# Performance work log

Hardware: AMD Instinct MI355X
Metric: run time of the kernel (lower is better)

The kernel has to match this reference:

```python
import jax, jax.numpy as jnp
import numpy as np

H = 64
NUM_HEADS = 4
NUM_LAYERS = 2
B = 524288
EPS = 1e-5


def _layernorm(x, g, b):
    mu = jnp.mean(x, axis=-1, keepdims=True)
    var = jnp.mean((x - mu) ** 2, axis=-1, keepdims=True)
    return (x - mu) * jax.lax.rsqrt(var + EPS) * g + b


def _mha(x, w_qkv, b_qkv, w_o, b_o):
    # x: (B, M, H). Fused in-proj like torch nn.MultiheadAttention.
    Bx, M, Hx = x.shape
    hd = Hx // NUM_HEADS
    qkv = x @ w_qkv.T + b_qkv                      # (B, M, 3H)
    q, k, v = jnp.split(qkv, 3, axis=-1)
    q = q.reshape(Bx, M, NUM_HEADS, hd)
    k = k.reshape(Bx, M, NUM_HEADS, hd)
    v = v.reshape(Bx, M, NUM_HEADS, hd)
    scores = jnp.einsum('bqnd,bknd->bnqk', q, k) / jnp.sqrt(jnp.asarray(hd, x.dtype))
    a = jax.nn.softmax(scores, axis=-1)
    o = jnp.einsum('bnqk,bknd->bqnd', a, v).reshape(Bx, M, Hx)
    return o @ w_o.T + b_o


def _block(x, rel, p):
    attn_out = _mha(x, p['w_qkv'], p['b_qkv'], p['w_o'], p['b_o'])
    attn_out = attn_out * rel[:, :, None]
    x = _layernorm(x + attn_out, p['n1_g'], p['n1_b'])
    ffn = jax.nn.relu(x @ p['ffn_w'].T + p['ffn_b'])
    return _layernorm(x + ffn, p['n2_g'], p['n2_b'])


def setup_inputs() -> dict:
    key = jax.random.key(0)
    ks = jax.random.split(key, 32)
    inp = {
        'h_poi': jax.random.normal(ks[0], (B, H), jnp.float32),
        'h_census': jax.random.normal(ks[1], (B, H), jnp.float32),
        'h_traffic': jax.random.normal(ks[2], (B, H), jnp.float32),
        'mfr_poi': jax.random.uniform(ks[3], (B, 2), jnp.float32),
        'mfr_census': jax.random.uniform(ks[4], (B, 2), jnp.float32),
        'mfr_traffic': jax.random.uniform(ks[5], (B, 2), jnp.float32),
        'rel_w': jax.random.normal(ks[6], (1, 2), jnp.float32) * 0.5,
        'rel_b': jnp.zeros((1,), jnp.float32),
    }
    s = 1.0 / np.sqrt(H)
    for l in range(NUM_LAYERS):
        kk = jax.random.split(ks[7 + l], 6)
        inp[f'l{l}_w_qkv'] = jax.random.normal(kk[0], (3 * H, H), jnp.float32) * s
        inp[f'l{l}_b_qkv'] = jnp.zeros((3 * H,), jnp.float32)
        inp[f'l{l}_w_o'] = jax.random.normal(kk[1], (H, H), jnp.float32) * s
        inp[f'l{l}_b_o'] = jnp.zeros((H,), jnp.float32)
        inp[f'l{l}_ffn_w'] = jax.random.normal(kk[2], (H, H), jnp.float32) * s
        inp[f'l{l}_ffn_b'] = jnp.zeros((H,), jnp.float32)
        inp[f'l{l}_n1_g'] = jnp.ones((H,), jnp.float32)
        inp[f'l{l}_n1_b'] = jnp.zeros((H,), jnp.float32)
        inp[f'l{l}_n2_g'] = jnp.ones((H,), jnp.float32)
        inp[f'l{l}_n2_b'] = jnp.zeros((H,), jnp.float32)
    return inp


def reference(h_poi, h_census, h_traffic, mfr_poi, mfr_census, mfr_traffic,
              rel_w, rel_b,
              l0_w_qkv, l0_b_qkv, l0_w_o, l0_b_o, l0_ffn_w, l0_ffn_b,
              l0_n1_g, l0_n1_b, l0_n2_g, l0_n2_b,
              l1_w_qkv, l1_b_qkv, l1_w_o, l1_b_o, l1_ffn_w, l1_ffn_b,
              l1_n1_g, l1_n1_b, l1_n2_g, l1_n2_b):
    x = jnp.stack([h_poi, h_census, h_traffic], axis=1)  # (B, 3, H)
    rel = jax.nn.sigmoid(
        jnp.stack([mfr_poi, mfr_census, mfr_traffic], axis=1) @ rel_w.T + rel_b
    )[..., 0]                                            # (B, 3)
    layers = [
        dict(w_qkv=l0_w_qkv, b_qkv=l0_b_qkv, w_o=l0_w_o, b_o=l0_b_o,
             ffn_w=l0_ffn_w, ffn_b=l0_ffn_b, n1_g=l0_n1_g, n1_b=l0_n1_b,
             n2_g=l0_n2_g, n2_b=l0_n2_b),
        dict(w_qkv=l1_w_qkv, b_qkv=l1_b_qkv, w_o=l1_w_o, b_o=l1_b_o,
             ffn_w=l1_ffn_w, ffn_b=l1_ffn_b, n1_g=l1_n1_g, n1_b=l1_n1_b,
             n2_g=l1_n2_g, n2_b=l1_n2_b),
    ]
    for p in layers:
        x = _block(x, rel, p)
    return x  # (B, 3, H); slice [:, i, :] per modality if dict output desired
```

## Files before the change

### kernel.cpp

```cpp
#include <hip/hip_runtime.h>

typedef unsigned short u16;
typedef unsigned int u32;
typedef _Float16 h16;
typedef h16 v8h __attribute__((ext_vector_type(8)));
typedef float v4f __attribute__((ext_vector_type(4)));

#define ROWS_PB 16
#define TOK 48
#define XS 76
#define AS 70
#define WS_L 20480

struct Params {
  const float *h0, *h1, *h2;
  const float *m0, *m1, *m2;
  const float *relw, *relb;
  const float *b_qkv[2], *b_o[2], *b_f[2];
  const float *n1g[2], *n1b[2], *n2g[2], *n2b[2];
  const u16* ws;
  float* out;
};

__device__ __forceinline__ u16 f2h(float f){ union{h16 h; u16 u;} c; c.h = (h16)f; return c.u; }

union Frag { uint2 u2[2]; uint4 u4; v8h v; };
union U2H  { uint2 u; h16 s[4]; };

__global__ __launch_bounds__(256, 2)
void prep_w(const float* wq0, const float* wo0, const float* wf0,
            const float* wq1, const float* wo1, const float* wf1, u16* ws){
  int idx = blockIdx.x * 256 + threadIdx.x;
  if (idx >= 2 * WS_L) return;
  int l = idx / WS_L, rem = idx % WS_L;
  const float* W; int loc;
  if (rem < 12288)      { W = l ? wq1 : wq0; loc = rem; }
  else if (rem < 16384) { W = l ? wo1 : wo0; loc = rem - 12288; }
  else                  { W = l ? wf1 : wf0; loc = rem - 16384; }
  int e = loc & 7, lane = (loc >> 3) & 63, fk = loc >> 9;
  int kk = fk & 1, nt = fk >> 1;
  int k = kk * 32 + 4 * (lane >> 4) + (e & 3) + (e >> 2) * 16;
  int n = nt * 16 + (lane & 15);
  ws[idx] = f2h(W[n * 64 + k]);
}

__device__ __forceinline__ v8h ldA(const u16* ap){
  Frag f;
  f.u2[0] = *(const uint2*)(ap);
  f.u2[1] = *(const uint2*)(ap + 16);
  return f.v;
}

__global__ __launch_bounds__(256, 5)
void inter_encoder(Params p){
  __shared__ u16  sX[TOK * XS];
  __shared__ u16  sATT[TOK * AS];
  __shared__ float sRel[TOK];

  const int tid  = threadIdx.x;
  const int lane = tid & 63, wv = tid >> 6;
  const int n15  = lane & 15, g = lane >> 4;
  const long long rowBase = (long long)blockIdx.x * ROWS_PB;

#pragma unroll
  for (int it = 0; it < 3; ++it){
    int idx = it * 256 + tid;
    int t = idx >> 4, c4 = (idx & 15) * 4;
    int r = t / 3, m = t - 3 * r;
    const float* hp = (m == 0) ? p.h0 : (m == 1) ? p.h1 : p.h2;
    float4 vv = *(const float4*)(hp + (rowBase + r) * 64 + c4);
    u32 lo = (u32)f2h(vv.x) | ((u32)f2h(vv.y) << 16);
    u32 hi = (u32)f2h(vv.z) | ((u32)f2h(vv.w) << 16);
    *(uint2*)(sX + t * XS + c4) = make_uint2(lo, hi);
  }
  if (tid < TOK){
    int r = tid / 3, m = tid - 3 * r;
    const float* mf = (m == 0) ? p.m0 : (m == 1) ? p.m1 : p.m2;
    float a0 = mf[(rowBase + r) * 2 + 0], a1 = mf[(rowBase + r) * 2 + 1];
    float z = a0 * p.relw[0] + a1 * p.relw[1] + p.relb[0];
    sRel[tid] = 1.f / (1.f + __expf(-z));
  }
  __syncthreads();

  for (int l = 0; l < 2; ++l){
    const u16* wsl = p.ws + l * WS_L;

    Frag aq[3][2];
    v4f bq4[3];
#pragma unroll
    for (int c = 0; c < 3; ++c){
      int mt = 4 * c + wv;
      aq[c][0].u4 = *(const uint4*)(wsl + ((mt * 2 + 0) * 64 + lane) * 8);
      aq[c][1].u4 = *(const uint4*)(wsl + ((mt * 2 + 1) * 64 + lane) * 8);
      bq4[c] = *(const v4f*)(p.b_qkv[l] + 16 * mt + 4 * g);
    }
    v4f acc[3][3];
#pragma unroll
    for (int m = 0; m < 3; ++m){
      const u16* bp = sX + (3 * n15 + m) * XS + 4 * g;
      v8h b0 = ldA(bp), b1 = ldA(bp + 32);
#pragma unroll
      for (int c = 0; c < 3; ++c){
        acc[c][m] = bq4[c];
        acc[c][m] = __builtin_amdgcn_mfma_f32_16x16x32_f16(aq[c][0].v, b0, acc[c][m], 0, 0, 0);
        acc[c][m] = __builtin_amdgcn_mfma_f32_16x16x32_f16(aq[c][1].v, b1, acc[c][m], 0, 0, 0);
      }
    }

    float s[3][3];
#pragma unroll
    for (int m1 = 0; m1 < 3; ++m1)
#pragma unroll
      for (int m2 = 0; m2 < 3; ++m2){
        float pp = acc[0][m1][0] * acc[1][m2][0]
                 + acc[0][m1][1] * acc[1][m2][1]
                 + acc[0][m1][2] * acc[1][m2][2]
                 + acc[0][m1][3] * acc[1][m2][3];
        pp += __shfl_xor(pp, 16, 64);
        pp += __shfl_xor(pp, 32, 64);
        s[m1][m2] = pp * 0.25f;
      }
#pragma unroll
    for (int m1 = 0; m1 < 3; ++m1){
      float mx = fmaxf(fmaxf(s[m1][0], s[m1][1]), s[m1][2]);
      float e0 = __expf(s[m1][0] - mx), e1 = __expf(s[m1][1] - mx), e2 = __expf(s[m1][2] - mx);
      float inv = 1.f / (e0 + e1 + e2);
      float a0 = e0 * inv, a1 = e1 * inv, a2 = e2 * inv;
      float o0 = a0 * acc[2][0][0] + a1 * acc[2][1][0] + a2 * acc[2][2][0];
      float o1 = a0 * acc[2][0][1] + a1 * acc[2][1][1] + a2 * acc[2][2][1];
      float o2 = a0 * acc[2][0][2] + a1 * acc[2][1][2] + a2 * acc[2][2][2];
      float o3 = a0 * acc[2][0][3] + a1 * acc[2][1][3] + a2 * acc[2][2][3];
      u32 lo = (u32)f2h(o0) | ((u32)f2h(o1) << 16);
      u32 hi = (u32)f2h(o2) | ((u32)f2h(o3) << 16);
      *(uint2*)(sATT + (3 * n15 + m1) * AS + 16 * wv + 4 * g) = make_uint2(lo, hi);
    }
    __syncthreads();

    if (wv < 3){
      const int c = 16 * wv + n15;
      const float relt = sRel[c];
      const u16* bp = sATT + c * AS + 4 * g;
      v8h b0 = ldA(bp), b1 = ldA(bp + 32);

      float val[4][4];
      float psum = 0.f, psq = 0.f;
#pragma unroll
      for (int j = 0; j < 4; ++j){
        Frag a0, a1;
        a0.u4 = *(const uint4*)(wsl + 12288 + ((j * 2 + 0) * 64 + lane) * 8);
        a1.u4 = *(const uint4*)(wsl + 12288 + ((j * 2 + 1) * 64 + lane) * 8);
        v4f acc2 = *(const v4f*)(p.b_o[l] + 16 * j + 4 * g);
        acc2 = __builtin_amdgcn_mfma_f32_16x16x32_f16(a0.v, b0, acc2, 0, 0, 0);
        acc2 = __builtin_amdgcn_mfma_f32_16x16x32_f16(a1.v, b1, acc2, 0, 0, 0);
        U2H x; x.u = *(const uint2*)(sX + c * XS + 16 * j + 4 * g);
#pragma unroll
        for (int i = 0; i < 4; ++i){
          float v = fmaf(acc2[i], relt, (float)x.s[i]);
          val[j][i] = v;
          psum += v;
          psq = fmaf(v, v, psq);
        }
      }
      psum += __shfl_xor(psum, 16, 64);
      psum += __shfl_xor(psum, 32, 64);
      psq  += __shfl_xor(psq, 16, 64);
      psq  += __shfl_xor(psq, 32, 64);
      float mu = psum * (1.f / 64.f);
      float rs = rsqrtf(fmaf(-mu, mu, psq * (1.f / 64.f)) + 1e-5f);

      float y[4][4];
#pragma unroll
      for (int j = 0; j < 4; ++j){
        v4f gg = *(const v4f*)(p.n1g[l] + 16 * j + 4 * g);
        v4f bb = *(const v4f*)(p.n1b[l] + 16 * j + 4 * g);
#pragma unroll
        for (int i = 0; i < 4; ++i) y[j][i] = (val[j][i] - mu) * rs * gg[i] + bb[i];
      }

      Frag c0, c1;
      c0.u4 = make_uint4((u32)f2h(y[0][0]) | ((u32)f2h(y[0][1]) << 16),
                         (u32)f2h(y[0][2]) | ((u32)f2h(y[0][3]) << 16),
                         (u32)f2h(y[1][0]) | ((u32)f2h(y[1][1]) << 16),
                         (u32)f2h(y[1][2]) | ((u32)f2h(y[1][3]) << 16));
      c1.u4 = make_uint4((u32)f2h(y[2][0]) | ((u32)f2h(y[2][1]) << 16),
                         (u32)f2h(y[2][2]) | ((u32)f2h(y[2][3]) << 16),
                         (u32)f2h(y[3][0]) | ((u32)f2h(y[3][1]) << 16),
                         (u32)f2h(y[3][2]) | ((u32)f2h(y[3][3]) << 16));

      float psum2 = 0.f, psq2 = 0.f;
#pragma unroll
      for (int j = 0; j < 4; ++j){
        Frag a0, a1;
        a0.u4 = *(const uint4*)(wsl + 16384 + ((j * 2 + 0) * 64 + lane) * 8);
        a1.u4 = *(const uint4*)(wsl + 16384 + ((j * 2 + 1) * 64 + lane) * 8);
        v4f acc2 = *(const v4f*)(p.b_f[l] + 16 * j + 4 * g);
        acc2 = __builtin_amdgcn_mfma_f32_16x16x32_f16(a0.v, c0.v, acc2, 0, 0, 0);
        acc2 = __builtin_amdgcn_mfma_f32_16x16x32_f16(a1.v, c1.v, acc2, 0, 0, 0);
#pragma unroll
        for (int i = 0; i < 4; ++i){
          float v2 = y[j][i] + fmaxf(acc2[i], 0.f);
          val[j][i] = v2;
          psum2 += v2;
          psq2 = fmaf(v2, v2, psq2);
        }
      }
      psum2 += __shfl_xor(psum2, 16, 64);
      psum2 += __shfl_xor(psum2, 32, 64);
      psq2  += __shfl_xor(psq2, 16, 64);
      psq2  += __shfl_xor(psq2, 32, 64);
      float mu2 = psum2 * (1.f / 64.f);
      float rs2 = rsqrtf(fmaf(-mu2, mu2, psq2 * (1.f / 64.f)) + 1e-5f);

      if (l == 0){
#pragma unroll
        for (int j = 0; j < 4; ++j){
          v4f gg = *(const v4f*)(p.n2g[0] + 16 * j + 4 * g);
          v4f bb = *(const v4f*)(p.n2b[0] + 16 * j + 4 * g);
          float z0 = (val[j][0] - mu2) * rs2 * gg[0] + bb[0];
          float z1 = (val[j][1] - mu2) * rs2 * gg[1] + bb[1];
          float z2 = (val[j][2] - mu2) * rs2 * gg[2] + bb[2];
          float z3 = (val[j][3] - mu2) * rs2 * gg[3] + bb[3];
          u32 lo = (u32)f2h(z0) | ((u32)f2h(z1) << 16);
          u32 hi = (u32)f2h(z2) | ((u32)f2h(z3) << 16);
          *(uint2*)(sX + c * XS + 16 * j + 4 * g) = make_uint2(lo, hi);
        }
      } else {
        float* op = p.out + (rowBase * 3 + c) * 64;
#pragma unroll
        for (int j = 0; j < 4; ++j){
          v4f gg = *(const v4f*)(p.n2g[1] + 16 * j + 4 * g);
          v4f bb = *(const v4f*)(p.n2b[1] + 16 * j + 4 * g);
          v4f yo;
#pragma unroll
          for (int i = 0; i < 4; ++i) yo[i] = (val[j][i] - mu2) * rs2 * gg[i] + bb[i];
          *(v4f*)(op + 16 * j + 4 * g) = yo;
        }
      }
    }
    __syncthreads();
  }
}

extern "C" void kernel_launch(void* const* d_in, const int* in_sizes, int n_in,
                              void* d_out, int out_size, void* d_ws, size_t ws_size,
                              hipStream_t stream){
  const float* const* in = (const float* const*)d_in;
  u16* ws = (u16*)d_ws;

  prep_w<<<(2 * WS_L + 255) / 256, 256, 0, stream>>>(
      in[8], in[10], in[12], in[18], in[20], in[22], ws);

  Params p;
  p.h0 = in[0]; p.h1 = in[1]; p.h2 = in[2];
  p.m0 = in[3]; p.m1 = in[4]; p.m2 = in[5];
  p.relw = in[6]; p.relb = in[7];
  for (int l = 0; l < 2; ++l){
    int b = 8 + 10 * l;
    p.b_qkv[l] = in[b + 1];
    p.b_o[l]   = in[b + 3];
    p.b_f[l]   = in[b + 5];
    p.n1g[l]   = in[b + 6]; p.n1b[l] = in[b + 7];
    p.n2g[l]   = in[b + 8]; p.n2b[l] = in[b + 9];
  }
  p.ws = ws;
  p.out = (float*)d_out;

  const int nblk = 524288 / ROWS_PB;
  inter_encoder<<<nblk, 256, 0, stream>>>(p);
}
```

Measured before the change: 483.0 us.

## Reorder token layout by modality, XOR-swizzle shared tiles, spread epilogue across all waves

Changes the shared-memory token ordering from row-interleaved to modality-major with an XOR swizzle on column groups, so that the global loads and the QKV B-fragment reads hit fewer LDS bank conflicts. The out-projection/LayerNorm/FFN epilogue now runs on all four waves with 12 tokens each (lanes past 47 clamp to a duplicate token) instead of three waves with 16 tokens each. The out-projection weight fragments are hoisted into registers before the softmax. The cost is extra register pressure from the hoisted fragments and redundant duplicate work and writes by the clamped lanes.

```diff
diff --git a/kernel.cpp b/kernel.cpp
--- a/kernel.cpp
+++ b/kernel.cpp
@@ -66,15 +66,15 @@
   for (int it = 0; it < 3; ++it){
     int idx = it * 256 + tid;
     int t = idx >> 4, c4 = (idx & 15) * 4;
-    int r = t / 3, m = t - 3 * r;
+    int m = t >> 4, r = t & 15;
     const float* hp = (m == 0) ? p.h0 : (m == 1) ? p.h1 : p.h2;
     float4 vv = *(const float4*)(hp + (rowBase + r) * 64 + c4);
     u32 lo = (u32)f2h(vv.x) | ((u32)f2h(vv.y) << 16);
     u32 hi = (u32)f2h(vv.z) | ((u32)f2h(vv.w) << 16);
-    *(uint2*)(sX + t * XS + c4) = make_uint2(lo, hi);
+    *(uint2*)(sX + t * XS + (c4 ^ (m << 2))) = make_uint2(lo, hi);
   }
   if (tid < TOK){
-    int r = tid / 3, m = tid - 3 * r;
+    int m = tid >> 4, r = tid & 15;
     const float* mf = (m == 0) ? p.m0 : (m == 1) ? p.m1 : p.m2;
     float a0 = mf[(rowBase + r) * 2 + 0], a1 = mf[(rowBase + r) * 2 + 1];
     float z = a0 * p.relw[0] + a1 * p.relw[1] + p.relb[0];
@@ -97,7 +97,7 @@
     v4f acc[3][3];
 #pragma unroll
     for (int m = 0; m < 3; ++m){
-      const u16* bp = sX + (3 * n15 + m) * XS + 4 * g;
+      const u16* bp = sX + (16 * m + n15) * XS + 4 * (g ^ m);
       v8h b0 = ldA(bp), b1 = ldA(bp + 32);
 #pragma unroll
       for (int c = 0; c < 3; ++c){
@@ -105,6 +105,13 @@
         acc[c][m] = __builtin_amdgcn_mfma_f32_16x16x32_f16(aq[c][0].v, b0, acc[c][m], 0, 0, 0);
         acc[c][m] = __builtin_amdgcn_mfma_f32_16x16x32_f16(aq[c][1].v, b1, acc[c][m], 0, 0, 0);
       }
+    }
+
+    Frag boA[4][2];
+#pragma unroll
+    for (int j = 0; j < 4; ++j){
+      boA[j][0].u4 = *(const uint4*)(wsl + 12288 + ((j * 2 + 0) * 64 + lane) * 8);
+      boA[j][1].u4 = *(const uint4*)(wsl + 12288 + ((j * 2 + 1) * 64 + lane) * 8);
     }
 
     float s[3][3];
@@ -132,27 +139,29 @@
       float o3 = a0 * acc[2][0][3] + a1 * acc[2][1][3] + a2 * acc[2][2][3];
       u32 lo = (u32)f2h(o0) | ((u32)f2h(o1) << 16);
       u32 hi = (u32)f2h(o2) | ((u32)f2h(o3) << 16);
-      *(uint2*)(sATT + (3 * n15 + m1) * AS + 16 * wv + 4 * g) = make_uint2(lo, hi);
+      *(uint2*)(sATT + (16 * m1 + n15) * AS + 16 * wv + 4 * g) = make_uint2(lo, hi);
     }
     __syncthreads();
 
-    if (wv < 3){
-      const int c = 16 * wv + n15;
-      const float relt = sRel[c];
-      const u16* bp = sATT + c * AS + 4 * g;
+    {
+      const int cc0 = 12 * wv + n15;
+      const int c = cc0 > 47 ? 47 : cc0;
+      const int r = (c * 171) >> 9;
+      const int m = c - 3 * r;
+      const int row = 16 * m + r;
+      const int gx = 4 * (g ^ m);
+      const float relt = sRel[row];
+      const u16* bp = sATT + row * AS + 4 * g;
       v8h b0 = ldA(bp), b1 = ldA(bp + 32);
 
       float val[4][4];
       float psum = 0.f, psq = 0.f;
 #pragma unroll
       for (int j = 0; j < 4; ++j){
-        Frag a0, a1;
-        a0.u4 = *(const uint4*)(wsl + 12288 + ((j * 2 + 0) * 64 + lane) * 8);
-        a1.u4 = *(const uint4*)(wsl + 12288 + ((j * 2 + 1) * 64 + lane) * 8);
         v4f acc2 = *(const v4f*)(p.b_o[l] + 16 * j + 4 * g);
-        acc2 = __builtin_amdgcn_mfma_f32_16x16x32_f16(a0.v, b0, acc2, 0, 0, 0);
-        acc2 = __builtin_amdgcn_mfma_f32_16x16x32_f16(a1.v, b1, acc2, 0, 0, 0);
-        U2H x; x.u = *(const uint2*)(sX + c * XS + 16 * j + 4 * g);
+        acc2 = __builtin_amdgcn_mfma_f32_16x16x32_f16(boA[j][0].v, b0, acc2, 0, 0, 0);
+        acc2 = __builtin_amdgcn_mfma_f32_16x16x32_f16(boA[j][1].v, b1, acc2, 0, 0, 0);
+        U2H x; x.u = *(const uint2*)(sX + row * XS + 16 * j + gx);
 #pragma unroll
         for (int i = 0; i < 4; ++i){
           float v = fmaf(acc2[i], relt, (float)x.s[i]);
@@ -222,7 +231,7 @@
           float z3 = (val[j][3] - mu2) * rs2 * gg[3] + bb[3];
           u32 lo = (u32)f2h(z0) | ((u32)f2h(z1) << 16);
           u32 hi = (u32)f2h(z2) | ((u32)f2h(z3) << 16);
-          *(uint2*)(sX + c * XS + 16 * j + 4 * g) = make_uint2(lo, hi);
+          *(uint2*)(sX + row * XS + 16 * j + gx) = make_uint2(lo, hi);
         }
       } else {
         float* op = p.out + (rowBase * 3 + c) * 64;
```

After: 516.4 us. 1.07x slower.
